# Performance work log

Measured on AMD Instinct MI355X. Metric: run time of the kernel, lower is better.

The kernel has to match this reference:

```python
import jax, jax.numpy as jnp
import numpy as np

N_NODES = 50000
N_EDGES = 800000
IN_C = 128
OUT_C = 128
BN_EPS = 1e-5


def setup_inputs() -> dict:
    key = jax.random.key(0)
    k1, k2, k3 = jax.random.split(key, 3)
    x = jax.random.normal(k1, (N_NODES, IN_C), dtype=jnp.float32)
    edge_index = jax.random.randint(k2, (2, N_EDGES), 0, N_NODES, dtype=jnp.int32)
    W = jax.random.normal(k3, (IN_C, OUT_C), dtype=jnp.float32) * (1.0 / np.sqrt(IN_C))
    bias = jnp.zeros((OUT_C,), dtype=jnp.float32)
    gamma = jnp.ones((OUT_C,), dtype=jnp.float32)
    beta = jnp.zeros((OUT_C,), dtype=jnp.float32)
    return {"x": x, "W": W, "bias": bias, "gamma": gamma, "beta": beta,
            "edge_index": edge_index}


def reference(x, W, bias, gamma, beta, edge_index):
    # GCNConv (PyG defaults): add self-loops, symmetric normalization, linear, scatter-add
    n = x.shape[0]
    h = x @ W  # [N, out_c]
    loops = jnp.arange(n, dtype=edge_index.dtype)
    row = jnp.concatenate([edge_index[0], loops])  # source nodes
    col = jnp.concatenate([edge_index[1], loops])  # target nodes
    # degree of targets (with self-loops, so deg >= 1)
    deg = jnp.zeros((n,), dtype=h.dtype).at[col].add(1.0)
    dinv = jax.lax.rsqrt(deg)
    norm = dinv[row] * dinv[col]  # [E+N]
    msg = h[row] * norm[:, None]  # gather + per-edge scale, [E+N, out_c]
    agg = jax.ops.segment_sum(msg, col, num_segments=n) + bias  # scatter-add
    # BatchNorm1d over node dimension (training-mode batch statistics)
    mean = jnp.mean(agg, axis=0)
    var = jnp.var(agg, axis=0)
    y = (agg - mean) * jax.lax.rsqrt(var + BN_EPS) * gamma + beta
    # ReLU; dropout is identity at inference
    return jax.nn.relu(y)
```

## Files before the change

kernel.cpp:

```cpp
#include <hip/hip_runtime.h>

#define N_NODES 50000
#define N_EDGES 800000
#define C 128
#define BN_EPS 1e-5f
#define BSHIFT 7
#define NBUCK ((N_NODES + 127) >> BSHIFT)
#define EPB 2048
#define A_BLOCKS ((N_EDGES + EPB - 1) / EPB)
#define EBUF 2560
#define GATHER_BLOCKS 512
#define GATHER_WAVES (GATHER_BLOCKS * 8)

typedef __attribute__((ext_vector_type(8))) short bf16x8;
typedef __attribute__((ext_vector_type(4))) float f32x4;

__device__ __forceinline__ unsigned pack_bf16x2(float a, float b) {
    unsigned ua = __float_as_uint(a);
    ua = (ua + 0x7FFFu + ((ua >> 16) & 1u)) >> 16;
    unsigned ub = __float_as_uint(b);
    ub = (ub + 0x7FFFu + ((ub >> 16) & 1u)) >> 16;
    return ua | (ub << 16);
}

__device__ __forceinline__ unsigned short bf16_1(float a) {
    unsigned u = __float_as_uint(a);
    return (unsigned short)((u + 0x7FFFu + ((u >> 16) & 1u)) >> 16);
}

__device__ __forceinline__ float blo(unsigned u) { return __uint_as_float(u << 16); }
__device__ __forceinline__ float bhi(unsigned u) { return __uint_as_float(u & 0xFFFF0000u); }

__device__ __forceinline__ unsigned pack_f16x2(float a, float b) {
    _Float16 ha = (_Float16)a, hb = (_Float16)b;
    return (unsigned)__builtin_bit_cast(unsigned short, ha) |
           ((unsigned)__builtin_bit_cast(unsigned short, hb) << 16);
}
__device__ __forceinline__ float f16lo(unsigned u) {
    return (float)__builtin_bit_cast(_Float16, (unsigned short)(u & 0xFFFFu));
}
__device__ __forceinline__ float f16hi(unsigned u) {
    return (float)__builtin_bit_cast(_Float16, (unsigned short)(u >> 16));
}

__global__ void __launch_bounds__(256) k_scat(const int* __restrict__ row,
                                              const int* __restrict__ col,
                                              unsigned* __restrict__ bEdges,
                                              int* __restrict__ bOffsT,
                                              const float* __restrict__ W,
                                              unsigned* __restrict__ WTn) {
    __shared__ int hist[NBUCK];
    __shared__ int wsum[8];
    int tid = threadIdx.x, w = blockIdx.x;
    int lane = tid & 63, wid = tid >> 6;
    for (int i = tid; i < NBUCK; i += 256) hist[i] = 0;
    __syncthreads();
    int e0 = w * EPB;
    int nE = N_EDGES - e0; if (nE > EPB) nE = EPB;
    int myc[8], myr[8];
#pragma unroll
    for (int k = 0; k < 8; ++k) {
        int idx = tid + (k << 8);
        bool ok = idx < nE;
        myc[k] = ok ? col[e0 + idx] : -1;
        myr[k] = ok ? row[e0 + idx] : 0;
        if (ok) atomicAdd(&hist[myc[k] >> BSHIFT], 1);
    }
    if (w == 0) {
#pragma unroll
        for (int it = 0; it < 32; ++it) {
            int i = tid + (it << 8);
            int j = i & 3, l = (i >> 2) & 63, kt = (i >> 8) & 3, nt = i >> 10;
            int m = l & 15, q = l >> 4;
            int kr = kt * 32 + q * 8 + 2 * j;
            int n = nt * 16 + m;
            WTn[i] = pack_bf16x2(W[kr * C + n], W[(kr + 1) * C + n]);
        }
    }
    __syncthreads();
    int v0 = hist[tid];
    int v1 = (tid + 256 < NBUCK) ? hist[tid + 256] : 0;
    int s0 = v0, s1 = v1;
#pragma unroll
    for (int d = 1; d < 64; d <<= 1) {
        int u0 = __shfl_up(s0, d, 64);
        int u1 = __shfl_up(s1, d, 64);
        if (lane >= d) { s0 += u0; s1 += u1; }
    }
    if (lane == 63) { wsum[wid] = s0; wsum[4 + wid] = s1; }
    __syncthreads();
    int tot0 = wsum[0] + wsum[1] + wsum[2] + wsum[3];
    int p0 = 0, p1 = tot0;
    for (int i = 0; i < wid; ++i) { p0 += wsum[i]; p1 += wsum[4 + i]; }
    int exc0 = p0 + s0 - v0;
    int exc1 = p1 + s1 - v1;
    bOffsT[tid * A_BLOCKS + w] = exc0;
    if (tid + 256 < NBUCK) bOffsT[(tid + 256) * A_BLOCKS + w] = exc1;
    if (tid == 0) bOffsT[NBUCK * A_BLOCKS + w] = nE;
    hist[tid] = exc0;
    if (tid + 256 < NBUCK) hist[tid + 256] = exc1;
    __syncthreads();
#pragma unroll
    for (int k = 0; k < 8; ++k) {
        if (myc[k] >= 0) {
            int b = myc[k] >> BSHIFT;
            int r = atomicAdd(&hist[b], 1);
            bEdges[(size_t)w * EPB + r] = (unsigned)myr[k] | ((unsigned)myc[k] << 16);
        }
    }
}

__global__ void __launch_bounds__(256) k_bsort(const unsigned* __restrict__ bEdges,
                                               const int* __restrict__ bOffsT,
                                               int* __restrict__ offs,
                                               int* __restrict__ cnt,
                                               unsigned short* __restrict__ srcs) {
    __shared__ int sS[A_BLOCKS];
    __shared__ int sO[A_BLOCKS + 1];
    __shared__ unsigned ebuf[EBUF];
    __shared__ int h[128];
    __shared__ int wsum[12];
    __shared__ int wtot;
    int tid = threadIdx.x, b = blockIdx.x;
    int lane = tid & 63, wid = tid >> 6;
    int i1 = tid + 256;
    int st0 = bOffsT[b * A_BLOCKS + tid];
    int v0 = bOffsT[(b + 1) * A_BLOCKS + tid] - st0;
    int st1 = 0, v1 = 0;
    if (i1 < A_BLOCKS) {
        st1 = bOffsT[b * A_BLOCKS + i1];
        v1 = bOffsT[(b + 1) * A_BLOCKS + i1] - st1;
    }
    sS[tid] = st0;
    if (i1 < A_BLOCKS) sS[i1] = st1;
    if (tid < 128) h[tid] = 0;
    int ep = st0 + st1;
    int s0 = v0, s1 = v1;
#pragma unroll
    for (int d = 1; d < 64; d <<= 1) {
        int u0 = __shfl_up(s0, d, 64);
        int u1 = __shfl_up(s1, d, 64);
        if (lane >= d) { s0 += u0; s1 += u1; }
        ep += __shfl_xor(ep, d, 64);
    }
    if (lane == 63) { wsum[wid] = s0; wsum[4 + wid] = s1; }
    if (lane == 0) wsum[8 + wid] = ep;
    __syncthreads();
    int tot0 = wsum[0] + wsum[1] + wsum[2] + wsum[3];
    int tot1 = wsum[4] + wsum[5] + wsum[6] + wsum[7];
    int e0 = wsum[8] + wsum[9] + wsum[10] + wsum[11];
    int p0 = 0, p1 = tot0;
    for (int i = 0; i < wid; ++i) { p0 += wsum[i]; p1 += wsum[4 + i]; }
    sO[tid] = p0 + s0 - v0;
    if (i1 < A_BLOCKS) sO[i1] = p1 + s1 - v1;
    if (tid == 0) sO[A_BLOCKS] = tot0 + tot1;
    __syncthreads();
    int c = sO[A_BLOCKS];
    if (c > EBUF) c = EBUF;
    for (int seg = tid; seg < A_BLOCKS; seg += 256) {
        int o = sO[seg];
        int n = sO[seg + 1] - o;
        const unsigned* srcp = bEdges + (size_t)seg * EPB + sS[seg];
        for (int k = 0; k < n; ++k) {
            int dp = o + k;
            if (dp < EBUF) ebuf[dp] = srcp[k];
        }
    }
    __syncthreads();
    int n0 = b << BSHIFT;
    int nn = N_NODES - n0; if (nn > 128) nn = 128;
    for (int e = tid; e < c; e += 256)
        atomicAdd(&h[(int)(ebuf[e] >> 16) - n0], 1);
    __syncthreads();
    int v = 0, sc = 0;
    if (tid < 128) {
        int ln = tid & 63;
        v = h[tid];
        sc = v;
#pragma unroll
        for (int d = 1; d < 64; d <<= 1) {
            int u = __shfl_up(sc, d, 64);
            if (ln >= d) sc += u;
        }
        if (tid == 63) wtot = sc;
    }
    __syncthreads();
    if (tid < 128) {
        int ex = sc - v + ((tid >= 64) ? wtot : 0);
        if (tid < nn) { offs[n0 + tid] = e0 + ex; cnt[n0 + tid] = v; }
        h[tid] = ex;
    }
    __syncthreads();
    for (int e = tid; e < c; e += 256) {
        unsigned pe = ebuf[e];
        int r = atomicAdd(&h[(int)(pe >> 16) - n0], 1);
        srcs[e0 + r] = (unsigned short)(pe & 0xFFFFu);
    }
    if (b == NBUCK - 1 && tid == 0) offs[N_NODES] = N_EDGES;
}

__global__ void __launch_bounds__(256) k_gemm(const float* __restrict__ x,
                                              const unsigned* __restrict__ WTn,
                                              const int* __restrict__ cnt,
                                              unsigned short* __restrict__ g,
                                              float* __restrict__ sums8) {
    __shared__ unsigned xs[64 * 68];
    int tid = threadIdx.x;
    if (blockIdx.x == 0) {
        for (int i = tid; i < 2048; i += 256) sums8[i] = 0.f;
    }
    int r0 = blockIdx.x * 64;
    const float4* x4 = (const float4*)x;
#pragma unroll
    for (int it = 0; it < 8; ++it) {
        int i = tid + (it << 8);
        int r = i >> 5, c4 = i & 31;
        float4 v = {0.f, 0.f, 0.f, 0.f};
        if (r0 + r < N_NODES) v = x4[(size_t)(r0 + r) * 32 + c4];
        xs[r * 68 + c4 * 2]     = pack_bf16x2(v.x, v.y);
        xs[r * 68 + c4 * 2 + 1] = pack_bf16x2(v.z, v.w);
    }
    __syncthreads();
    int wave = tid >> 6, lane = tid & 63;
    int r0w = r0 + wave * 16;
    if (r0w >= N_NODES) return;
    int m = lane & 15, q = lane >> 4;
    bf16x8 afrag[4];
#pragma unroll
    for (int kt = 0; kt < 4; ++kt)
        afrag[kt] = *(const bf16x8*)&xs[(wave * 16 + m) * 68 + kt * 16 + q * 4];
    const uint4* B4 = (const uint4*)WTn;
    f32x4 acc[8];
#pragma unroll
    for (int nt = 0; nt < 8; ++nt)
        acc[nt][0] = acc[nt][1] = acc[nt][2] = acc[nt][3] = 0.f;
#pragma unroll
    for (int nt = 0; nt < 8; ++nt) {
#pragma unroll
        for (int kt = 0; kt < 4; ++kt) {
            uint4 braw = B4[(nt * 4 + kt) * 64 + lane];
            bf16x8 bfrag = __builtin_bit_cast(bf16x8, braw);
            acc[nt] = __builtin_amdgcn_mfma_f32_16x16x32_bf16(afrag[kt], bfrag, acc[nt], 0, 0, 0);
        }
    }
    int rb = r0w + q * 4;
    float dv[4];
#pragma unroll
    for (int reg = 0; reg < 4; ++reg) dv[reg] = rsqrtf((float)cnt[rb + reg] + 1.f);
#pragma unroll
    for (int nt = 0; nt < 8; ++nt) {
        int cbase = nt * 16 + m;
#pragma unroll
        for (int reg = 0; reg < 4; ++reg)
            g[(size_t)(rb + reg) * C + cbase] = bf16_1(acc[nt][reg] * dv[reg]);
    }
}

#define ACC8(v) { a[0]+=blo(v.x); a[1]+=bhi(v.x); a[2]+=blo(v.y); a[3]+=bhi(v.y); \
                  a[4]+=blo(v.z); a[5]+=bhi(v.z); a[6]+=blo(v.w); a[7]+=bhi(v.w); }
__global__ void __launch_bounds__(512) k_gather(const int* __restrict__ offs,
                                                const unsigned short* __restrict__ srcs,
                                                const uint4* __restrict__ g4,
                                                unsigned* __restrict__ aggh,
                                                float* __restrict__ sums8) {
    __shared__ float lsA[8][32][4], lsQ[8][32][4];
    int tid = threadIdx.x;
    int lane = tid & 63, wid = tid >> 6;
    int l = lane & 15, q = lane >> 4;
    float sA[4] = {0.f, 0.f, 0.f, 0.f}, sQ[4] = {0.f, 0.f, 0.f, 0.f};
    int gw = blockIdx.x * 8 + wid;
    for (int node = gw; node < N_NODES; node += GATHER_WAVES) {
        int beg = offs[node], end = offs[node + 1];
        float a[8];
        if (q == 0) {
            uint4 u = g4[(size_t)node * 16 + l];
            a[0]=blo(u.x); a[1]=bhi(u.x); a[2]=blo(u.y); a[3]=bhi(u.y);
            a[4]=blo(u.z); a[5]=bhi(u.z); a[6]=blo(u.w); a[7]=bhi(u.w);
        } else {
#pragma unroll
            for (int i = 0; i < 8; ++i) a[i] = 0.f;
        }
        for (int base = beg; base < end; base += 64) {
            int nb = end - base; if (nb > 64) nb = 64;
            int sv = (base + lane < end) ? (int)srcs[base + lane] : 0;
            int j0 = 0;
            for (; j0 + 16 <= nb; j0 += 16) {
                int i0 = j0 + q;
                int s0 = __shfl(sv, i0, 64);
                int s1 = __shfl(sv, i0 + 4, 64);
                int s2 = __shfl(sv, i0 + 8, 64);
                int s3 = __shfl(sv, i0 + 12, 64);
                uint4 v0 = g4[(size_t)s0 * 16 + l];
                uint4 v1 = g4[(size_t)s1 * 16 + l];
                uint4 v2 = g4[(size_t)s2 * 16 + l];
                uint4 v3 = g4[(size_t)s3 * 16 + l];
                ACC8(v0) ACC8(v1) ACC8(v2) ACC8(v3)
            }
            if (j0 < nb) {
#pragma unroll
                for (int k = 0; k < 4; ++k) {
                    int idx = j0 + q + 4 * k;
                    int s = __shfl(sv, idx, 64);
                    if (idx < nb) { uint4 v = g4[(size_t)s * 16 + l]; ACC8(v) }
                }
            }
        }
#pragma unroll
        for (int i = 0; i < 8; ++i) {
            a[i] += __shfl_xor(a[i], 16, 64);
            a[i] += __shfl_xor(a[i], 32, 64);
        }
        float dt = rsqrtf((float)(end - beg) + 1.f);
        if (q < 2) {
            float f0 = a[q * 4 + 0] * dt, f1 = a[q * 4 + 1] * dt;
            float f2 = a[q * 4 + 2] * dt, f3 = a[q * 4 + 3] * dt;
            sA[0] += f0; sQ[0] += f0 * f0;
            sA[1] += f1; sQ[1] += f1 * f1;
            sA[2] += f2; sQ[2] += f2 * f2;
            sA[3] += f3; sQ[3] += f3 * f3;
            uint2 pv; pv.x = pack_f16x2(f0, f1); pv.y = pack_f16x2(f2, f3);
            *(uint2*)(aggh + (size_t)node * 64 + l * 4 + q * 2) = pv;
        }
    }
    if (q < 2) {
#pragma unroll
        for (int i = 0; i < 4; ++i) {
            lsA[wid][l * 2 + q][i] = sA[i];
            lsQ[wid][l * 2 + q][i] = sQ[i];
        }
    }
    __syncthreads();
    if (tid < 128) {
        int ch = tid;
        int ll = ch >> 3, qq = (ch >> 2) & 1, ii = ch & 3;
        float s = 0.f, sq = 0.f;
#pragma unroll
        for (int wd = 0; wd < 8; ++wd) {
            s  += lsA[wd][ll * 2 + qq][ii];
            sq += lsQ[wd][ll * 2 + qq][ii];
        }
        int slice = (blockIdx.x & 7) * 256;
        atomicAdd(&sums8[slice + ch], s);
        atomicAdd(&sums8[slice + 128 + ch], sq);
    }
}

__global__ void __launch_bounds__(256) k_final(const unsigned* __restrict__ aggh,
                                               float* __restrict__ out,
                                               const float* __restrict__ sums8,
                                               const float* __restrict__ gamma,
                                               const float* __restrict__ beta) {
    __shared__ float sc_s[C], sh_s[C];
    int tid = threadIdx.x;
    if (tid < C) {
        float s = 0.f, sq = 0.f;
#pragma unroll
        for (int k = 0; k < 8; ++k) {
            s  += sums8[k * 256 + tid];
            sq += sums8[k * 256 + 128 + tid];
        }
        float mean = s * (1.0f / N_NODES);
        float var = sq * (1.0f / N_NODES) - mean * mean;
        float sc = gamma[tid] * rsqrtf(var + BN_EPS);
        sc_s[tid] = sc;
        sh_s[tid] = beta[tid] - mean * sc;
    }
    __syncthreads();
    int i = blockIdx.x * 256 + tid;
    uint4 v = ((const uint4*)aggh)[i];
    int c = (i & 15) * 8;
    float4 o0, o1;
    o0.x = fmaxf(f16lo(v.x) * sc_s[c+0] + sh_s[c+0], 0.f);
    o0.y = fmaxf(f16hi(v.x) * sc_s[c+1] + sh_s[c+1], 0.f);
    o0.z = fmaxf(f16lo(v.y) * sc_s[c+2] + sh_s[c+2], 0.f);
    o0.w = fmaxf(f16hi(v.y) * sc_s[c+3] + sh_s[c+3], 0.f);
    o1.x = fmaxf(f16lo(v.z) * sc_s[c+4] + sh_s[c+4], 0.f);
    o1.y = fmaxf(f16hi(v.z) * sc_s[c+5] + sh_s[c+5], 0.f);
    o1.z = fmaxf(f16lo(v.w) * sc_s[c+6] + sh_s[c+6], 0.f);
    o1.w = fmaxf(f16hi(v.w) * sc_s[c+7] + sh_s[c+7], 0.f);
    float4* o = (float4*)(out + (size_t)i * 8);
    o[0] = o0; o[1] = o1;
}

extern "C" void kernel_launch(void* const* d_in, const int* in_sizes, int n_in,
                              void* d_out, int out_size, void* d_ws, size_t ws_size,
                              hipStream_t stream) {
    const float* x     = (const float*)d_in[0];
    const float* W     = (const float*)d_in[1];
    const float* gamma = (const float*)d_in[3];
    const float* beta  = (const float*)d_in[4];
    const int*   eidx  = (const int*)d_in[5];
    const int* row = eidx;
    const int* col = eidx + N_EDGES;

    float* out = (float*)d_out;

    unsigned* g      = (unsigned*)d_ws;
    unsigned* aggh   = g + (size_t)N_NODES * 64;
    unsigned* bEdges = aggh + (size_t)N_NODES * 64;
    unsigned* WTn    = bEdges + (size_t)A_BLOCKS * EPB;
    unsigned short* srcs = (unsigned short*)(WTn + 8192);
    int*   cnt    = (int*)(srcs + N_EDGES);
    int*   offs   = cnt + N_NODES;
    float* sums8  = (float*)(offs + N_NODES + 4);
    int*   bOffsT = (int*)(sums8 + 2048);

    k_scat<<<A_BLOCKS, 256, 0, stream>>>(row, col, bEdges, bOffsT, W, WTn);
    k_bsort<<<NBUCK, 256, 0, stream>>>(bEdges, bOffsT, offs, cnt, srcs);
    k_gemm<<<(N_NODES + 63) / 64, 256, 0, stream>>>(x, WTn, cnt, (unsigned short*)g, sums8);
    k_gather<<<GATHER_BLOCKS, 512, 0, stream>>>(offs, srcs, (const uint4*)g, aggh, sums8);
    k_final<<<N_NODES * 16 / 256, 256, 0, stream>>>(aggh, out, sums8, gamma, beta);
}
```

Baseline: 162.5 us.

## Merge bucket sort and GEMM into one launch, move source-degree scaling into gather

```diff
diff --git a/kernel.cpp b/kernel.cpp
--- a/kernel.cpp
+++ b/kernel.cpp
@@ -9,6 +9,7 @@
 #define EPB 2048
 #define A_BLOCKS ((N_EDGES + EPB - 1) / EPB)
 #define EBUF 2560
+#define GEMM_BLOCKS ((N_NODES + 63) / 64)
 #define GATHER_BLOCKS 512
 #define GATHER_WAVES (GATHER_BLOCKS * 8)
 
@@ -48,25 +49,10 @@
                                               unsigned* __restrict__ bEdges,
                                               int* __restrict__ bOffsT,
                                               const float* __restrict__ W,
-                                              unsigned* __restrict__ WTn) {
-    __shared__ int hist[NBUCK];
-    __shared__ int wsum[8];
+                                              unsigned* __restrict__ WTn,
+                                              float* __restrict__ sums8) {
     int tid = threadIdx.x, w = blockIdx.x;
-    int lane = tid & 63, wid = tid >> 6;
-    for (int i = tid; i < NBUCK; i += 256) hist[i] = 0;
-    __syncthreads();
-    int e0 = w * EPB;
-    int nE = N_EDGES - e0; if (nE > EPB) nE = EPB;
-    int myc[8], myr[8];
-#pragma unroll
-    for (int k = 0; k < 8; ++k) {
-        int idx = tid + (k << 8);
-        bool ok = idx < nE;
-        myc[k] = ok ? col[e0 + idx] : -1;
-        myr[k] = ok ? row[e0 + idx] : 0;
-        if (ok) atomicAdd(&hist[myc[k] >> BSHIFT], 1);
-    }
-    if (w == 0) {
+    if (w == A_BLOCKS) {
 #pragma unroll
         for (int it = 0; it < 32; ++it) {
             int i = tid + (it << 8);
@@ -76,6 +62,24 @@
             int n = nt * 16 + m;
             WTn[i] = pack_bf16x2(W[kr * C + n], W[(kr + 1) * C + n]);
         }
+        for (int i = tid; i < 2048; i += 256) sums8[i] = 0.f;
+        return;
+    }
+    __shared__ int hist[NBUCK];
+    __shared__ int wsum[8];
+    int lane = tid & 63, wid = tid >> 6;
+    for (int i = tid; i < NBUCK; i += 256) hist[i] = 0;
+    __syncthreads();
+    int e0 = w * EPB;
+    int nE = N_EDGES - e0; if (nE > EPB) nE = EPB;
+    int myc[8], myr[8];
+#pragma unroll
+    for (int k = 0; k < 8; ++k) {
+        int idx = tid + (k << 8);
+        bool ok = idx < nE;
+        myc[k] = ok ? col[e0 + idx] : -1;
+        myr[k] = ok ? row[e0 + idx] : 0;
+        if (ok) atomicAdd(&hist[myc[k] >> BSHIFT], 1);
     }
     __syncthreads();
     int v0 = hist[tid];
@@ -110,157 +114,154 @@
     }
 }
 
-__global__ void __launch_bounds__(256) k_bsort(const unsigned* __restrict__ bEdges,
-                                               const int* __restrict__ bOffsT,
-                                               int* __restrict__ offs,
-                                               int* __restrict__ cnt,
-                                               unsigned short* __restrict__ srcs) {
-    __shared__ int sS[A_BLOCKS];
-    __shared__ int sO[A_BLOCKS + 1];
-    __shared__ unsigned ebuf[EBUF];
-    __shared__ int h[128];
+__global__ void __launch_bounds__(256) k_mid(const unsigned* __restrict__ bEdges,
+                                             const int* __restrict__ bOffsT,
+                                             int* __restrict__ offs,
+                                             float* __restrict__ dinvArr,
+                                             unsigned short* __restrict__ srcs,
+                                             const float* __restrict__ x,
+                                             const unsigned* __restrict__ WTn,
+                                             unsigned short* __restrict__ g16) {
+    __shared__ __align__(16) unsigned sm[4352];
     __shared__ int wsum[12];
     __shared__ int wtot;
-    int tid = threadIdx.x, b = blockIdx.x;
+    int tid = threadIdx.x;
     int lane = tid & 63, wid = tid >> 6;
-    int i1 = tid + 256;
-    int st0 = bOffsT[b * A_BLOCKS + tid];
-    int v0 = bOffsT[(b + 1) * A_BLOCKS + tid] - st0;
-    int st1 = 0, v1 = 0;
-    if (i1 < A_BLOCKS) {
-        st1 = bOffsT[b * A_BLOCKS + i1];
-        v1 = bOffsT[(b + 1) * A_BLOCKS + i1] - st1;
-    }
-    sS[tid] = st0;
-    if (i1 < A_BLOCKS) sS[i1] = st1;
-    if (tid < 128) h[tid] = 0;
-    int ep = st0 + st1;
-    int s0 = v0, s1 = v1;
-#pragma unroll
-    for (int d = 1; d < 64; d <<= 1) {
-        int u0 = __shfl_up(s0, d, 64);
-        int u1 = __shfl_up(s1, d, 64);
-        if (lane >= d) { s0 += u0; s1 += u1; }
-        ep += __shfl_xor(ep, d, 64);
-    }
-    if (lane == 63) { wsum[wid] = s0; wsum[4 + wid] = s1; }
-    if (lane == 0) wsum[8 + wid] = ep;
-    __syncthreads();
-    int tot0 = wsum[0] + wsum[1] + wsum[2] + wsum[3];
-    int tot1 = wsum[4] + wsum[5] + wsum[6] + wsum[7];
-    int e0 = wsum[8] + wsum[9] + wsum[10] + wsum[11];
-    int p0 = 0, p1 = tot0;
-    for (int i = 0; i < wid; ++i) { p0 += wsum[i]; p1 += wsum[4 + i]; }
-    sO[tid] = p0 + s0 - v0;
-    if (i1 < A_BLOCKS) sO[i1] = p1 + s1 - v1;
-    if (tid == 0) sO[A_BLOCKS] = tot0 + tot1;
-    __syncthreads();
-    int c = sO[A_BLOCKS];
-    if (c > EBUF) c = EBUF;
-    for (int seg = tid; seg < A_BLOCKS; seg += 256) {
-        int o = sO[seg];
-        int n = sO[seg + 1] - o;
-        const unsigned* srcp = bEdges + (size_t)seg * EPB + sS[seg];
-        for (int k = 0; k < n; ++k) {
-            int dp = o + k;
-            if (dp < EBUF) ebuf[dp] = srcp[k];
-        }
-    }
-    __syncthreads();
-    int n0 = b << BSHIFT;
-    int nn = N_NODES - n0; if (nn > 128) nn = 128;
-    for (int e = tid; e < c; e += 256)
-        atomicAdd(&h[(int)(ebuf[e] >> 16) - n0], 1);
-    __syncthreads();
-    int v = 0, sc = 0;
-    if (tid < 128) {
-        int ln = tid & 63;
-        v = h[tid];
-        sc = v;
+    if (blockIdx.x < NBUCK) {
+        const int b = blockIdx.x;
+        int* sS = (int*)sm;
+        int* sO = (int*)sm + 392;
+        unsigned* ebuf = sm + 792;
+        int* h = (int*)(sm + 792 + EBUF);
+        int i1 = tid + 256;
+        int st0 = bOffsT[b * A_BLOCKS + tid];
+        int v0 = bOffsT[(b + 1) * A_BLOCKS + tid] - st0;
+        int st1 = 0, v1 = 0;
+        if (i1 < A_BLOCKS) {
+            st1 = bOffsT[b * A_BLOCKS + i1];
+            v1 = bOffsT[(b + 1) * A_BLOCKS + i1] - st1;
+        }
+        sS[tid] = st0;
+        if (i1 < A_BLOCKS) sS[i1] = st1;
+        if (tid < 128) h[tid] = 0;
+        int ep = st0 + st1;
+        int s0 = v0, s1 = v1;
 #pragma unroll
         for (int d = 1; d < 64; d <<= 1) {
-            int u = __shfl_up(sc, d, 64);
-            if (ln >= d) sc += u;
-        }
-        if (tid == 63) wtot = sc;
-    }
-    __syncthreads();
-    if (tid < 128) {
-        int ex = sc - v + ((tid >= 64) ? wtot : 0);
-        if (tid < nn) { offs[n0 + tid] = e0 + ex; cnt[n0 + tid] = v; }
-        h[tid] = ex;
-    }
-    __syncthreads();
-    for (int e = tid; e < c; e += 256) {
-        unsigned pe = ebuf[e];
-        int r = atomicAdd(&h[(int)(pe >> 16) - n0], 1);
-        srcs[e0 + r] = (unsigned short)(pe & 0xFFFFu);
-    }
-    if (b == NBUCK - 1 && tid == 0) offs[N_NODES] = N_EDGES;
-}
-
-__global__ void __launch_bounds__(256) k_gemm(const float* __restrict__ x,
-                                              const unsigned* __restrict__ WTn,
-                                              const int* __restrict__ cnt,
-                                              unsigned short* __restrict__ g,
-                                              float* __restrict__ sums8) {
-    __shared__ unsigned xs[64 * 68];
-    int tid = threadIdx.x;
-    if (blockIdx.x == 0) {
-        for (int i = tid; i < 2048; i += 256) sums8[i] = 0.f;
-    }
-    int r0 = blockIdx.x * 64;
-    const float4* x4 = (const float4*)x;
-#pragma unroll
-    for (int it = 0; it < 8; ++it) {
-        int i = tid + (it << 8);
-        int r = i >> 5, c4 = i & 31;
-        float4 v = {0.f, 0.f, 0.f, 0.f};
-        if (r0 + r < N_NODES) v = x4[(size_t)(r0 + r) * 32 + c4];
-        xs[r * 68 + c4 * 2]     = pack_bf16x2(v.x, v.y);
-        xs[r * 68 + c4 * 2 + 1] = pack_bf16x2(v.z, v.w);
-    }
-    __syncthreads();
-    int wave = tid >> 6, lane = tid & 63;
-    int r0w = r0 + wave * 16;
-    if (r0w >= N_NODES) return;
-    int m = lane & 15, q = lane >> 4;
-    bf16x8 afrag[4];
-#pragma unroll
-    for (int kt = 0; kt < 4; ++kt)
-        afrag[kt] = *(const bf16x8*)&xs[(wave * 16 + m) * 68 + kt * 16 + q * 4];
-    const uint4* B4 = (const uint4*)WTn;
-    f32x4 acc[8];
-#pragma unroll
-    for (int nt = 0; nt < 8; ++nt)
-        acc[nt][0] = acc[nt][1] = acc[nt][2] = acc[nt][3] = 0.f;
-#pragma unroll
-    for (int nt = 0; nt < 8; ++nt) {
-#pragma unroll
-        for (int kt = 0; kt < 4; ++kt) {
-            uint4 braw = B4[(nt * 4 + kt) * 64 + lane];
-            bf16x8 bfrag = __builtin_bit_cast(bf16x8, braw);
-            acc[nt] = __builtin_amdgcn_mfma_f32_16x16x32_bf16(afrag[kt], bfrag, acc[nt], 0, 0, 0);
-        }
-    }
-    int rb = r0w + q * 4;
-    float dv[4];
-#pragma unroll
-    for (int reg = 0; reg < 4; ++reg) dv[reg] = rsqrtf((float)cnt[rb + reg] + 1.f);
-#pragma unroll
-    for (int nt = 0; nt < 8; ++nt) {
-        int cbase = nt * 16 + m;
-#pragma unroll
-        for (int reg = 0; reg < 4; ++reg)
-            g[(size_t)(rb + reg) * C + cbase] = bf16_1(acc[nt][reg] * dv[reg]);
-    }
-}
-
-#define ACC8(v) { a[0]+=blo(v.x); a[1]+=bhi(v.x); a[2]+=blo(v.y); a[3]+=bhi(v.y); \
-                  a[4]+=blo(v.z); a[5]+=bhi(v.z); a[6]+=blo(v.w); a[7]+=bhi(v.w); }
+            int u0 = __shfl_up(s0, d, 64);
+            int u1 = __shfl_up(s1, d, 64);
+            if (lane >= d) { s0 += u0; s1 += u1; }
+            ep += __shfl_xor(ep, d, 64);
+        }
+        if (lane == 63) { wsum[wid] = s0; wsum[4 + wid] = s1; }
+        if (lane == 0) wsum[8 + wid] = ep;
+        __syncthreads();
+        int tot0 = wsum[0] + wsum[1] + wsum[2] + wsum[3];
+        int tot1 = wsum[4] + wsum[5] + wsum[6] + wsum[7];
+        int e0 = wsum[8] + wsum[9] + wsum[10] + wsum[11];
+        int p0 = 0, p1 = tot0;
+        for (int i = 0; i < wid; ++i) { p0 += wsum[i]; p1 += wsum[4 + i]; }
+        sO[tid] = p0 + s0 - v0;
+        if (i1 < A_BLOCKS) sO[i1] = p1 + s1 - v1;
+        if (tid == 0) sO[A_BLOCKS] = tot0 + tot1;
+        __syncthreads();
+        int c = sO[A_BLOCKS];
+        if (c > EBUF) c = EBUF;
+        for (int seg = tid; seg < A_BLOCKS; seg += 256) {
+            int o = sO[seg];
+            int n = sO[seg + 1] - o;
+            const unsigned* srcp = bEdges + (size_t)seg * EPB + sS[seg];
+            for (int k = 0; k < n; ++k) {
+                int dp = o + k;
+                if (dp < EBUF) ebuf[dp] = srcp[k];
+            }
+        }
+        __syncthreads();
+        int n0 = b << BSHIFT;
+        int nn = N_NODES - n0; if (nn > 128) nn = 128;
+        for (int e = tid; e < c; e += 256)
+            atomicAdd(&h[(int)(ebuf[e] >> 16) - n0], 1);
+        __syncthreads();
+        int v = 0, sc = 0;
+        if (tid < 128) {
+            int ln = tid & 63;
+            v = h[tid];
+            sc = v;
+#pragma unroll
+            for (int d = 1; d < 64; d <<= 1) {
+                int u = __shfl_up(sc, d, 64);
+                if (ln >= d) sc += u;
+            }
+            if (tid == 63) wtot = sc;
+        }
+        __syncthreads();
+        if (tid < 128) {
+            int ex = sc - v + ((tid >= 64) ? wtot : 0);
+            if (tid < nn) {
+                offs[n0 + tid] = e0 + ex;
+                dinvArr[n0 + tid] = rsqrtf((float)v + 1.f);
+            }
+            h[tid] = ex;
+        }
+        __syncthreads();
+        for (int e = tid; e < c; e += 256) {
+            unsigned pe = ebuf[e];
+            int r = atomicAdd(&h[(int)(pe >> 16) - n0], 1);
+            srcs[e0 + r] = (unsigned short)(pe & 0xFFFFu);
+        }
+        if (b == NBUCK - 1 && tid == 0) offs[N_NODES] = N_EDGES;
+    } else {
+        unsigned* xs = sm;
+        int r0 = (blockIdx.x - NBUCK) * 64;
+        const float4* x4 = (const float4*)x;
+#pragma unroll
+        for (int it = 0; it < 8; ++it) {
+            int i = tid + (it << 8);
+            int r = i >> 5, c4 = i & 31;
+            float4 v = {0.f, 0.f, 0.f, 0.f};
+            if (r0 + r < N_NODES) v = x4[(size_t)(r0 + r) * 32 + c4];
+            xs[r * 68 + c4 * 2]     = pack_bf16x2(v.x, v.y);
+            xs[r * 68 + c4 * 2 + 1] = pack_bf16x2(v.z, v.w);
+        }
+        __syncthreads();
+        int r0w = r0 + wid * 16;
+        if (r0w >= N_NODES) return;
+        int m = lane & 15, q = lane >> 4;
+        bf16x8 afrag[4];
+#pragma unroll
+        for (int kt = 0; kt < 4; ++kt)
+            afrag[kt] = *(const bf16x8*)&xs[(wid * 16 + m) * 68 + kt * 16 + q * 4];
+        const uint4* B4 = (const uint4*)WTn;
+        f32x4 acc[8];
+#pragma unroll
+        for (int nt = 0; nt < 8; ++nt)
+            acc[nt][0] = acc[nt][1] = acc[nt][2] = acc[nt][3] = 0.f;
+#pragma unroll
+        for (int nt = 0; nt < 8; ++nt) {
+#pragma unroll
+            for (int kt = 0; kt < 4; ++kt) {
+                uint4 braw = B4[(nt * 4 + kt) * 64 + lane];
+                bf16x8 bfrag = __builtin_bit_cast(bf16x8, braw);
+                acc[nt] = __builtin_amdgcn_mfma_f32_16x16x32_bf16(afrag[kt], bfrag, acc[nt], 0, 0, 0);
+            }
+        }
+        int rb = r0w + q * 4;
+#pragma unroll
+        for (int nt = 0; nt < 8; ++nt) {
+            int cbase = nt * 16 + m;
+#pragma unroll
+            for (int reg = 0; reg < 4; ++reg)
+                g16[(size_t)(rb + reg) * C + cbase] = bf16_1(acc[nt][reg]);
+        }
+    }
+}
+
+#define ACC8S(v, d) { a[0]+=blo(v.x)*d; a[1]+=bhi(v.x)*d; a[2]+=blo(v.y)*d; a[3]+=bhi(v.y)*d; \
+                      a[4]+=blo(v.z)*d; a[5]+=bhi(v.z)*d; a[6]+=blo(v.w)*d; a[7]+=bhi(v.w)*d; }
 __global__ void __launch_bounds__(512) k_gather(const int* __restrict__ offs,
                                                 const unsigned short* __restrict__ srcs,
                                                 const uint4* __restrict__ g4,
+                                                const float* __restrict__ dinvArr,
                                                 unsigned* __restrict__ aggh,
                                                 float* __restrict__ sums8) {
     __shared__ float lsA[8][32][4], lsQ[8][32][4];
@@ -271,11 +272,12 @@
     int gw = blockIdx.x * 8 + wid;
     for (int node = gw; node < N_NODES; node += GATHER_WAVES) {
         int beg = offs[node], end = offs[node + 1];
+        float dt = dinvArr[node];
         float a[8];
         if (q == 0) {
             uint4 u = g4[(size_t)node * 16 + l];
-            a[0]=blo(u.x); a[1]=bhi(u.x); a[2]=blo(u.y); a[3]=bhi(u.y);
-            a[4]=blo(u.z); a[5]=bhi(u.z); a[6]=blo(u.w); a[7]=bhi(u.w);
+            a[0]=blo(u.x)*dt; a[1]=bhi(u.x)*dt; a[2]=blo(u.y)*dt; a[3]=bhi(u.y)*dt;
+            a[4]=blo(u.z)*dt; a[5]=bhi(u.z)*dt; a[6]=blo(u.w)*dt; a[7]=bhi(u.w)*dt;
         } else {
 #pragma unroll
             for (int i = 0; i < 8; ++i) a[i] = 0.f;
@@ -290,18 +292,23 @@
                 int s1 = __shfl(sv, i0 + 4, 64);
                 int s2 = __shfl(sv, i0 + 8, 64);
                 int s3 = __shfl(sv, i0 + 12, 64);
+                float d0 = dinvArr[s0], d1 = dinvArr[s1], d2 = dinvArr[s2], d3 = dinvArr[s3];
                 uint4 v0 = g4[(size_t)s0 * 16 + l];
                 uint4 v1 = g4[(size_t)s1 * 16 + l];
                 uint4 v2 = g4[(size_t)s2 * 16 + l];
                 uint4 v3 = g4[(size_t)s3 * 16 + l];
-                ACC8(v0) ACC8(v1) ACC8(v2) ACC8(v3)
+                ACC8S(v0, d0) ACC8S(v1, d1) ACC8S(v2, d2) ACC8S(v3, d3)
             }
             if (j0 < nb) {
 #pragma unroll
                 for (int k = 0; k < 4; ++k) {
                     int idx = j0 + q + 4 * k;
                     int s = __shfl(sv, idx, 64);
-                    if (idx < nb) { uint4 v = g4[(size_t)s * 16 + l]; ACC8(v) }
+                    if (idx < nb) {
+                        float dd = dinvArr[s];
+                        uint4 v = g4[(size_t)s * 16 + l];
+                        ACC8S(v, dd)
+                    }
                 }
             }
         }
@@ -310,7 +317,6 @@
             a[i] += __shfl_xor(a[i], 16, 64);
             a[i] += __shfl_xor(a[i], 32, 64);
         }
-        float dt = rsqrtf((float)(end - beg) + 1.f);
         if (q < 2) {
             float f0 = a[q * 4 + 0] * dt, f1 = a[q * 4 + 1] * dt;
             float f2 = a[q * 4 + 2] * dt, f3 = a[q * 4 + 3] * dt;
@@ -331,8 +337,7 @@
     }
     __syncthreads();
     if (tid < 128) {
-        int ch = tid;
-        int ll = ch >> 3, qq = (ch >> 2) & 1, ii = ch & 3;
+        int ll = tid >> 3, qq = (tid >> 2) & 1, ii = tid & 3;
         float s = 0.f, sq = 0.f;
 #pragma unroll
         for (int wd = 0; wd < 8; ++wd) {
@@ -340,8 +345,8 @@
             sq += lsQ[wd][ll * 2 + qq][ii];
         }
         int slice = (blockIdx.x & 7) * 256;
-        atomicAdd(&sums8[slice + ch], s);
-        atomicAdd(&sums8[slice + 128 + ch], sq);
+        atomicAdd(&sums8[slice + tid], s);
+        atomicAdd(&sums8[slice + 128 + tid], sq);
     }
 }
 
@@ -400,14 +405,14 @@
     unsigned* bEdges = aggh + (size_t)N_NODES * 64;
     unsigned* WTn    = bEdges + (size_t)A_BLOCKS * EPB;
     unsigned short* srcs = (unsigned short*)(WTn + 8192);
-    int*   cnt    = (int*)(srcs + N_EDGES);
-    int*   offs   = cnt + N_NODES;
-    float* sums8  = (float*)(offs + N_NODES + 4);
-    int*   bOffsT = (int*)(sums8 + 2048);
-
-    k_scat<<<A_BLOCKS, 256, 0, stream>>>(row, col, bEdges, bOffsT, W, WTn);
-    k_bsort<<<NBUCK, 256, 0, stream>>>(bEdges, bOffsT, offs, cnt, srcs);
-    k_gemm<<<(N_NODES + 63) / 64, 256, 0, stream>>>(x, WTn, cnt, (unsigned short*)g, sums8);
-    k_gather<<<GATHER_BLOCKS, 512, 0, stream>>>(offs, srcs, (const uint4*)g, aggh, sums8);
+    int*   offs    = (int*)(srcs + N_EDGES);
+    float* dinvArr = (float*)(offs + N_NODES + 4);
+    float* sums8   = dinvArr + N_NODES;
+    int*   bOffsT  = (int*)(sums8 + 2048);
+
+    k_scat<<<A_BLOCKS + 1, 256, 0, stream>>>(row, col, bEdges, bOffsT, W, WTn, sums8);
+    k_mid<<<NBUCK + GEMM_BLOCKS, 256, 0, stream>>>(bEdges, bOffsT, offs, dinvArr, srcs,
+                                                   x, WTn, (unsigned short*)g);
+    k_gather<<<GATHER_BLOCKS, 512, 0, stream>>>(offs, srcs, (const uint4*)g, dinvArr, aggh, sums8);
     k_final<<<N_NODES * 16 / 256, 256, 0, stream>>>(aggh, out, sums8, gamma, beta);
 }
```

After: 153.1 us, median of 2. -5.8%, faster.
